# Kernel tuning notes

Hardware: AMD Instinct MI355X
Metric: run time of the kernel (lower is better)

The kernel has to match this reference:

```python
import jax, jax.numpy as jnp
import numpy as np

N_NODES = 50000
N_EDGES = 800000
N_GRAPHS = 64
NUM_CLASSES = 10


def _glorot(key, shape):
    fan_in, fan_out = shape
    lim = np.sqrt(6.0 / (fan_in + fan_out)).astype(np.float32)
    return jax.random.uniform(key, shape, jnp.float32, -lim, lim)


def setup_inputs() -> dict:
    key = jax.random.key(0)
    ks = jax.random.split(key, 12)
    x = jax.random.normal(ks[0], (N_NODES, 5), jnp.float32)
    edge_index = jax.random.randint(ks[1], (2, N_EDGES), 0, N_NODES, jnp.int64)
    batch = jnp.sort(jax.random.randint(ks[2], (N_NODES,), 0, N_GRAPHS, jnp.int64))
    dims = [5, 32, 64, 128, 256]
    params = {}
    for i in range(4):
        params[f"W{i+1}"] = _glorot(ks[3 + i], (dims[i], dims[i + 1]))
        params[f"b{i+1}"] = jnp.zeros((dims[i + 1],), jnp.float32)
    params["fcW"] = _glorot(ks[7], (256, NUM_CLASSES))
    params["fcb"] = jnp.zeros((NUM_CLASSES,), jnp.float32)
    return {"x": x, "edge_index": edge_index, "batch": batch, **params}


def reference(x, edge_index, batch, W1, b1, W2, b2, W3, b3, W4, b4, fcW, fcb):
    n = x.shape[0]
    loop = jnp.arange(n, dtype=edge_index.dtype)
    src = jnp.concatenate([edge_index[0], loop])  # source nodes (+ self loops)
    dst = jnp.concatenate([edge_index[1], loop])  # target nodes (+ self loops)
    # symmetric GCN normalization: D^{-1/2} (A+I) D^{-1/2}
    deg = jax.ops.segment_sum(jnp.ones_like(dst, x.dtype), dst, num_segments=n)
    dinv = jax.lax.rsqrt(deg)  # deg >= 1 due to self loops
    norm = (dinv[src] * dinv[dst])[:, None]

    def gcn(h, W, b):
        h = h @ W                                        # dense transform
        agg = jax.ops.segment_sum(h[src] * norm, dst, num_segments=n)
        return agg + b

    h = jax.nn.relu(gcn(x, W1, b1))
    h = jax.nn.relu(gcn(h, W2, b2))
    h = jax.nn.relu(gcn(h, W3, b3))
    h = jax.nn.relu(gcn(h, W4, b4))                      # [n, 256]

    # global mean pool over graphs
    counts = jax.ops.segment_sum(jnp.ones((n,), h.dtype), batch, num_segments=N_GRAPHS)
    pooled = jax.ops.segment_sum(h, batch, num_segments=N_GRAPHS)
    pooled = pooled / jnp.maximum(counts, 1.0)[:, None]  # [G, 256]

    return jax.nn.log_softmax(pooled @ fcW + fcb, axis=-1)
```

## Files before the change

kernel.cpp:

```cpp
#include <hip/hip_runtime.h>
#include <hip/hip_bf16.h>
#include <math.h>

#define N_NODES 50000
#define N_EDGES 800000
#define N_GRAPHS 64
#define NUM_CLASSES 10
#define BIN_W 256
#define NBINS ((N_NODES + BIN_W - 1) / BIN_W)
#define CHUNK 4096
#define NCHUNKS ((N_EDGES + CHUNK - 1) / CHUNK)
#define CAP 8192
#define CPB 64
#define PACK_BLOCKS 11

typedef __attribute__((ext_vector_type(8))) short bf16x8;
typedef __attribute__((ext_vector_type(4))) float f32x4;

__device__ inline unsigned short f2bf(float f) {
    unsigned int u = __float_as_uint(f);
    u += 0x7fffu + ((u >> 16) & 1u);
    return (unsigned short)(u >> 16);
}
__device__ inline float bf2f(unsigned short v) {
    return __uint_as_float((unsigned int)v << 16);
}
__device__ inline void bf8_unpack(uint4 v, float* o) {
    o[0] = __uint_as_float(v.x << 16); o[1] = __uint_as_float(v.x & 0xffff0000u);
    o[2] = __uint_as_float(v.y << 16); o[3] = __uint_as_float(v.y & 0xffff0000u);
    o[4] = __uint_as_float(v.z << 16); o[5] = __uint_as_float(v.z & 0xffff0000u);
    o[6] = __uint_as_float(v.w << 16); o[7] = __uint_as_float(v.w & 0xffff0000u);
}
__device__ inline unsigned int pack2(float a, float b) {
    return (unsigned int)f2bf(a) | ((unsigned int)f2bf(b) << 16);
}

template<int K, int N>
__device__ void packW_dev(const float* __restrict__ W, unsigned short* __restrict__ Wp,
                          int bid, int l) {
    constexpr int KT = K / 32;
    int kt = bid % KT, nt = bid / KT;
    int m = l & 15, quad = l >> 4;
    #pragma unroll
    for (int j = 0; j < 8; j++) {
        int k = kt * 32 + quad * 8 + j;
        int n = nt * 16 + m;
        Wp[((size_t)bid * 64 + l) * 8 + j] = f2bf(W[(size_t)k * N + n]);
    }
}

__global__ __launch_bounds__(512) void k_binscatter(const int* __restrict__ src,
                                                    const int* __restrict__ dst,
                                                    unsigned short* __restrict__ cnt,
                                                    unsigned int* __restrict__ binned,
                                                    const float* __restrict__ W2,
                                                    const float* __restrict__ W3,
                                                    const float* __restrict__ W4,
                                                    unsigned short* wp2, unsigned short* wp3,
                                                    unsigned short* wp4) {
    int bid = blockIdx.x, t = threadIdx.x;
    if (bid >= NCHUNKS) {
        int w = (bid - NCHUNKS) * 8 + (t >> 6);
        int lane = t & 63;
        if (w < 4)       packW_dev<32, 64>(W2, wp2, w, lane);
        else if (w < 20) packW_dev<64, 128>(W3, wp3, w - 4, lane);
        else if (w < 84) packW_dev<128, 256>(W4, wp4, w - 20, lane);
        return;
    }
    __shared__ int hist[NBINS];
    __shared__ int off[NBINS];
    __shared__ int bump[NBINS];
    __shared__ unsigned int stage[CHUNK];
    __shared__ unsigned char sbin[CHUNK];
    __shared__ int ws8[8];
    int base = bid * CHUNK;
    int total = N_EDGES - base; if (total > CHUNK) total = CHUNK;
    for (int i = t; i < NBINS; i += 512) { hist[i] = 0; bump[i] = 0; }
    __syncthreads();
    int es[8], ed[8];
    #pragma unroll
    for (int i = 0; i < 8; i++) {
        int e = base + t + i * 512;
        if (e < N_EDGES) { es[i] = src[e]; ed[i] = dst[e]; }
        else ed[i] = -1;
    }
    #pragma unroll
    for (int i = 0; i < 8; i++)
        if (ed[i] >= 0) atomicAdd(&hist[ed[i] >> 8], 1);
    __syncthreads();
    {
        int v = (t < NBINS) ? hist[t] : 0;
        int h0 = v;
        int lane = t & 63, w = t >> 6;
        #pragma unroll
        for (int o = 1; o < 64; o <<= 1) { int u = __shfl_up(v, o); if (lane >= o) v += u; }
        if (lane == 63) ws8[w] = v;
        __syncthreads();
        int add = 0;
        #pragma unroll
        for (int i = 0; i < 8; i++) add += (i < w) ? ws8[i] : 0;
        if (t < NBINS) off[t] = v + add - h0;
        __syncthreads();
    }
    #pragma unroll
    for (int i = 0; i < 8; i++) {
        if (ed[i] >= 0) {
            int b = ed[i] >> 8;
            int lpos = off[b] + atomicAdd(&bump[b], 1);
            stage[lpos] = ((unsigned int)(ed[i] & 255) << 16) | (unsigned int)es[i];
            sbin[lpos] = (unsigned char)b;
        }
    }
    __syncthreads();
    for (int j = t; j < total; j += 512) {
        int b = sbin[j];
        int pos = j - off[b];
        if (pos < CPB)
            binned[((size_t)b * NCHUNKS + bid) * CPB + pos] = stage[j];
    }
    if (t < NBINS) {
        int h = hist[t]; if (h > CPB) h = CPB;
        cnt[(size_t)bid * NBINS + t] = (unsigned short)h;
    }
}

__global__ __launch_bounds__(512) void k_csr(const unsigned int* __restrict__ binned,
                                             const unsigned short* __restrict__ cnt,
                                             unsigned int* __restrict__ row_ptr,
                                             float* __restrict__ dinv,
                                             unsigned short* __restrict__ csr16,
                                             const float* __restrict__ x,
                                             float* __restrict__ x5) {
    __shared__ unsigned int stage[CAP];
    __shared__ int coff[256];
    __shared__ unsigned short mycs[256];
    __shared__ int deg[BIN_W];
    __shared__ int off[BIN_W];
    __shared__ int bump[BIN_W];
    __shared__ int ws8[8];
    __shared__ int s_total;
    int b = blockIdx.x;
    int t = threadIdx.x;
    if (t < BIN_W) { deg[t] = 0; bump[t] = 0; }
    int myc = (t < NCHUNKS) ? (int)cnt[(size_t)t * NBINS + b] : 0;
    {
        int v = myc;
        int lane = t & 63, w = t >> 6;
        #pragma unroll
        for (int o = 1; o < 64; o <<= 1) { int u = __shfl_up(v, o); if (lane >= o) v += u; }
        if (lane == 63) ws8[w] = v;
        __syncthreads();
        int add = 0;
        #pragma unroll
        for (int i = 0; i < 8; i++) add += (i < w) ? ws8[i] : 0;
        if (t < 256) { coff[t] = v + add - myc; mycs[t] = (unsigned short)myc; }
        if (t == 511) s_total = v + add;
        __syncthreads();
    }
    int total = s_total; if (total > CAP) total = CAP;
    for (int c = t >> 4; c < NCHUNKS; c += 32) {
        int mc = mycs[c];
        const unsigned int* seg = &binned[((size_t)b * NCHUNKS + c) * CPB];
        int o0 = coff[c];
        for (int j = t & 15; j < mc && o0 + j < CAP; j += 16)
            stage[o0 + j] = seg[j];
    }
    __syncthreads();
    for (int e = t; e < total; e += 512)
        atomicAdd(&deg[stage[e] >> 16], 1);
    __syncthreads();
    {
        int v = (t < BIN_W) ? deg[t] : 0;
        int d0 = v;
        int lane = t & 63, w = t >> 6;
        #pragma unroll
        for (int o = 1; o < 64; o <<= 1) { int u = __shfl_up(v, o); if (lane >= o) v += u; }
        if (lane == 63) ws8[w] = v;
        __syncthreads();
        int add = 0;
        #pragma unroll
        for (int i = 0; i < 8; i++) add += (i < w) ? ws8[i] : 0;
        if (t < BIN_W) off[t] = v + add - d0;
        __syncthreads();
    }
    int e0 = b * CAP;
    if (t < BIN_W) {
        int node = b * BIN_W + t;
        if (node < N_NODES) {
            float di = rsqrtf((float)(deg[t] + 1));
            row_ptr[node] = (unsigned int)(e0 + off[t]) | ((unsigned int)deg[t] << 21);
            dinv[node] = di;
            #pragma unroll
            for (int f = 0; f < 5; f++)
                x5[node * 5 + f] = di * x[node * 5 + f];
        }
    }
    for (int e = t; e < total; e += 512) {
        unsigned int v = stage[e];
        int dl = v >> 16;
        int pos = e0 + off[dl] + atomicAdd(&bump[dl], 1);
        csr16[pos] = (unsigned short)(v & 0xffffu);
    }
}

__global__ __launch_bounds__(256) void k_layer1(const float* __restrict__ x5,
                                                const unsigned int* __restrict__ row_ptr,
                                                const unsigned short* __restrict__ csr16,
                                                const float* __restrict__ dinv,
                                                const float* __restrict__ W1,
                                                const float* __restrict__ b1,
                                                unsigned short* __restrict__ Hout) {
    __shared__ float A5[32 * 6];
    __shared__ float Ws[160];
    __shared__ float bs[32];
    int t = threadIdx.x;
    int row0 = blockIdx.x * 32;
    if (t < 160) Ws[t] = W1[t];
    if (t >= 224) bs[t - 224] = b1[t - 224];
    int nl = t >> 3, f = t & 7;
    int node = row0 + nl;
    float val = 0.0f;
    float dnode = 0.0f;
    if (node < N_NODES) dnode = dinv[node];
    if (f < 5 && node < N_NODES) {
        float acc0 = x5[node * 5 + f], acc1 = 0.0f;
        unsigned int v = row_ptr[node];
        int e0 = (int)(v & 0x1FFFFFu);
        int e1 = e0 + (int)(v >> 21);
        int e = e0;
        for (; e + 7 < e1; e += 8) {
            int s0 = csr16[e], s1 = csr16[e + 1], s2 = csr16[e + 2], s3 = csr16[e + 3];
            int s4 = csr16[e + 4], s5 = csr16[e + 5], s6 = csr16[e + 6], s7 = csr16[e + 7];
            float x0 = x5[s0 * 5 + f], x1 = x5[s1 * 5 + f];
            float x2 = x5[s2 * 5 + f], x3 = x5[s3 * 5 + f];
            float x4 = x5[s4 * 5 + f], x5v = x5[s5 * 5 + f];
            float x6 = x5[s6 * 5 + f], x7 = x5[s7 * 5 + f];
            acc0 += (x0 + x2) + (x4 + x6);
            acc1 += (x1 + x3) + (x5v + x7);
        }
        for (; e + 3 < e1; e += 4) {
            int s0 = csr16[e], s1 = csr16[e + 1], s2 = csr16[e + 2], s3 = csr16[e + 3];
            float x0 = x5[s0 * 5 + f], x1 = x5[s1 * 5 + f];
            float x2 = x5[s2 * 5 + f], x3 = x5[s3 * 5 + f];
            acc0 += x0 + x2;
            acc1 += x1 + x3;
        }
        for (; e < e1; e++) acc0 += x5[csr16[e] * 5 + f];
        val = dnode * (acc0 + acc1);
    }
    if (f < 5) A5[nl * 6 + f] = val;
    __syncthreads();
    int j0 = (t & 7) * 4;
    int node2 = row0 + (t >> 3);
    float d2 = (node2 < N_NODES) ? dinv[node2] : 0.0f;
    float a[5];
    #pragma unroll
    for (int k = 0; k < 5; k++) a[k] = A5[(t >> 3) * 6 + k];
    ushort4 o;
    unsigned short* op = (unsigned short*)&o;
    #pragma unroll
    for (int c = 0; c < 4; c++) {
        float acc = bs[j0 + c];
        #pragma unroll
        for (int k = 0; k < 5; k++) acc += a[k] * Ws[k * 32 + j0 + c];
        op[c] = f2bf(d2 * fmaxf(acc, 0.0f));
    }
    if (node2 < N_NODES) *(ushort4*)&Hout[(size_t)node2 * 32 + j0] = o;
}

template<int K, int N, bool SCALE, bool POOL>
__global__ __launch_bounds__(256) void k_fused(const unsigned short* __restrict__ Hin,
                                               const unsigned int* __restrict__ row_ptr,
                                               const unsigned short* __restrict__ csr16,
                                               const float* __restrict__ dinv,
                                               const unsigned short* __restrict__ Wp,
                                               const float* __restrict__ bias,
                                               unsigned short* __restrict__ C,
                                               const int* __restrict__ batch,
                                               float* __restrict__ pooled) {
    constexpr int KT = K / 32, NT = N / 16, DV = K / 8;
    constexpr int NPB = 2048 / K;
    constexpr int TM = NPB / 16;
    constexpr int KP = K + 8;
    __shared__ unsigned short As[NPB * KP];
    __shared__ int bb[POOL ? NPB : 4];
    int t = threadIdx.x;
    int row0 = blockIdx.x * NPB;
    if constexpr (POOL) {
        if (t < NPB) bb[t] = batch[min(row0 + t, N_NODES - 1)];
    }
    {
        int nl = t / DV, f = t % DV;
        int node = row0 + nl;
        const uint4* h4 = (const uint4*)Hin;
        uint4 o = {0u, 0u, 0u, 0u};
        if (node < N_NODES) {
            float di = dinv[node];
            float acc0[8], acc1[8];
            bf8_unpack(h4[(size_t)node * DV + f], acc0);
            #pragma unroll
            for (int i = 0; i < 8; i++) acc1[i] = 0.0f;
            unsigned int rv = row_ptr[node];
            int e0 = (int)(rv & 0x1FFFFFu);
            int e1 = e0 + (int)(rv >> 21);
            int e = e0;
            for (; e + 3 < e1; e += 4) {
                int s0 = csr16[e], s1 = csr16[e + 1], s2 = csr16[e + 2], s3 = csr16[e + 3];
                uint4 u0 = h4[(size_t)s0 * DV + f];
                uint4 u1 = h4[(size_t)s1 * DV + f];
                uint4 u2 = h4[(size_t)s2 * DV + f];
                uint4 u3 = h4[(size_t)s3 * DV + f];
                float t0[8], t1[8], t2[8], t3[8];
                bf8_unpack(u0, t0); bf8_unpack(u1, t1);
                bf8_unpack(u2, t2); bf8_unpack(u3, t3);
                #pragma unroll
                for (int i = 0; i < 8; i++) {
                    acc0[i] += t0[i] + t2[i];
                    acc1[i] += t1[i] + t3[i];
                }
            }
            for (; e + 1 < e1; e += 2) {
                int s0 = csr16[e], s1 = csr16[e + 1];
                uint4 u0 = h4[(size_t)s0 * DV + f];
                uint4 u1 = h4[(size_t)s1 * DV + f];
                float t0[8], t1[8];
                bf8_unpack(u0, t0);
                bf8_unpack(u1, t1);
                #pragma unroll
                for (int i = 0; i < 8; i++) { acc0[i] += t0[i]; acc1[i] += t1[i]; }
            }
            if (e < e1) {
                float t0[8];
                bf8_unpack(h4[(size_t)csr16[e] * DV + f], t0);
                #pragma unroll
                for (int i = 0; i < 8; i++) acc0[i] += t0[i];
            }
            o.x = pack2(di * (acc0[0] + acc1[0]), di * (acc0[1] + acc1[1]));
            o.y = pack2(di * (acc0[2] + acc1[2]), di * (acc0[3] + acc1[3]));
            o.z = pack2(di * (acc0[4] + acc1[4]), di * (acc0[5] + acc1[5]));
            o.w = pack2(di * (acc0[6] + acc1[6]), di * (acc0[7] + acc1[7]));
        }
        *(uint4*)&As[nl * KP + f * 8] = o;
    }
    __syncthreads();
    int wave = t >> 6, lane = t & 63;
    int m = lane & 15, quad = lane >> 4;
    bf16x8 a[TM][KT];
    float dr[TM][4];
    #pragma unroll
    for (int mt = 0; mt < TM; mt++) {
        #pragma unroll
        for (int kt = 0; kt < KT; kt++)
            a[mt][kt] = *(const bf16x8*)&As[(mt * 16 + m) * KP + kt * 32 + quad * 8];
        #pragma unroll
        for (int r = 0; r < 4; r++) {
            int row = row0 + mt * 16 + quad * 4 + r;
            dr[mt][r] = (SCALE && row < N_NODES) ? dinv[row] : 1.0f;
        }
    }
    const bf16x8* Bp = (const bf16x8*)Wp;
    int g0 = 0, g1 = 0;
    if constexpr (POOL) { g0 = bb[0]; g1 = bb[NPB - 1]; }
    for (int j = wave; j < TM * NT; j += 4) {
        int mt = j % TM, nt = j / TM;
        f32x4 c = {0.f, 0.f, 0.f, 0.f};
        #pragma unroll
        for (int kt = 0; kt < KT; kt++)
            c = __builtin_amdgcn_mfma_f32_16x16x32_bf16(a[mt][kt],
                    Bp[(size_t)(nt * KT + kt) * 64 + lane], c, 0, 0, 0);
        int col = nt * 16 + m;
        float bv = bias[col];
        if constexpr (POOL) {
            float acc0 = 0.0f, acc1 = 0.0f;
            #pragma unroll
            for (int r = 0; r < 4; r++) {
                int rl = mt * 16 + quad * 4 + r;
                int row = row0 + rl;
                if (row < N_NODES) {
                    float v = fmaxf(c[r] + bv, 0.0f);
                    int g = bb[rl];
                    if (g == g0) acc0 += v;
                    else if (g == g1) acc1 += v;
                    else atomicAdd(&pooled[(size_t)g * 256 + col], v);
                }
            }
            acc0 += __shfl_xor(acc0, 32); acc0 += __shfl_xor(acc0, 16);
            acc1 += __shfl_xor(acc1, 32); acc1 += __shfl_xor(acc1, 16);
            if (lane < 16) {
                atomicAdd(&pooled[(size_t)g0 * 256 + col], acc0);
                if (g1 != g0) atomicAdd(&pooled[(size_t)g1 * 256 + col], acc1);
            }
        } else {
            #pragma unroll
            for (int r = 0; r < 4; r++) {
                int row = row0 + mt * 16 + quad * 4 + r;
                if (row < N_NODES) {
                    float v = fmaxf(c[r] + bv, 0.0f);
                    if constexpr (SCALE) v *= dr[mt][r];
                    C[(size_t)row * N + col] = f2bf(v);
                }
            }
        }
    }
}

__global__ void k_final(const float* __restrict__ pooled, const int* __restrict__ batch,
                        const float* __restrict__ fcW, const float* __restrict__ fcb,
                        float* __restrict__ out) {
    int g = blockIdx.x;
    int t = threadIdx.x;
    float cnt = 0.0f;
    if (t == 0) {
        int lo = 0, hi = N_NODES;
        while (lo < hi) { int m = (lo + hi) >> 1; if (batch[m] < g) lo = m + 1; else hi = m; }
        int start = lo;
        lo = 0; hi = N_NODES;
        while (lo < hi) { int m = (lo + hi) >> 1; if (batch[m] < g + 1) lo = m + 1; else hi = m; }
        cnt = (float)(lo - start);
    }
    float inv = 1.0f / fmaxf(__shfl(cnt, 0), 1.0f);
    float p[4];
    #pragma unroll
    for (int m = 0; m < 4; m++) p[m] = pooled[g * 256 + t + 64 * m];
    float logits[NUM_CLASSES];
    #pragma unroll
    for (int j = 0; j < NUM_CLASSES; j++) {
        float s = 0.0f;
        #pragma unroll
        for (int m = 0; m < 4; m++) s += p[m] * fcW[(t + 64 * m) * NUM_CLASSES + j];
        for (int off = 32; off > 0; off >>= 1) s += __shfl_xor(s, off);
        logits[j] = s * inv + fcb[j];
    }
    float mx = logits[0];
    #pragma unroll
    for (int j = 1; j < NUM_CLASSES; j++) mx = fmaxf(mx, logits[j]);
    float se = 0.0f;
    #pragma unroll
    for (int j = 0; j < NUM_CLASSES; j++) se += expf(logits[j] - mx);
    float lse = mx + logf(se);
    if (t < NUM_CLASSES) out[g * NUM_CLASSES + t] = logits[t] - lse;
}

extern "C" void kernel_launch(void* const* d_in, const int* in_sizes, int n_in,
                              void* d_out, int out_size, void* d_ws, size_t ws_size,
                              hipStream_t stream) {
    const float* x     = (const float*)d_in[0];
    const int*   ei    = (const int*)d_in[1];
    const int*   src   = ei;
    const int*   dst   = ei + N_EDGES;
    const int*   batch = (const int*)d_in[2];
    const float* W1 = (const float*)d_in[3];  const float* b1 = (const float*)d_in[4];
    const float* W2 = (const float*)d_in[5];  const float* b2 = (const float*)d_in[6];
    const float* W3 = (const float*)d_in[7];  const float* b3 = (const float*)d_in[8];
    const float* W4 = (const float*)d_in[9];  const float* b4 = (const float*)d_in[10];
    const float* fcW = (const float*)d_in[11]; const float* fcb = (const float*)d_in[12];
    float* out = (float*)d_out;

    char* ws = (char*)d_ws;
    unsigned short* buf1 = (unsigned short*)ws; ws += (size_t)N_NODES * 256 * 2;
    unsigned short* buf2 = (unsigned short*)ws; ws += (size_t)N_NODES * 256 * 2;
    float* dinv     = (float*)ws; ws += (size_t)N_NODES * 4;
    float* x5       = (float*)ws; ws += (size_t)N_NODES * 5 * 4 + 16;
    unsigned int* row_ptr = (unsigned int*)ws; ws += (size_t)(N_NODES + 4) * 4;
    unsigned short* csr16 = (unsigned short*)ws; ws += (size_t)NBINS * CAP * 2;
    unsigned int* binned = (unsigned int*)ws; ws += (size_t)NBINS * NCHUNKS * CPB * 4;
    unsigned short* cnt = (unsigned short*)ws; ws += (size_t)NCHUNKS * NBINS * 2 + 16;
    float* pooled   = (float*)ws; ws += (size_t)N_GRAPHS * 256 * 4;
    unsigned short* wp2 = (unsigned short*)ws; ws += 32 * 64 * 2;
    unsigned short* wp3 = (unsigned short*)ws; ws += 64 * 128 * 2;
    unsigned short* wp4 = (unsigned short*)ws; ws += 128 * 256 * 2;

    const int TB = 256;
    k_binscatter<<<NCHUNKS + PACK_BLOCKS, 512, 0, stream>>>(src, dst, cnt, binned,
                                                            W2, W3, W4, wp2, wp3, wp4);
    k_csr<<<NBINS, 512, 0, stream>>>(binned, cnt, row_ptr, dinv, csr16, x, x5);

    k_layer1<<<(N_NODES + 31) / 32, TB, 0, stream>>>(x5, row_ptr, csr16, dinv, W1, b1, buf1);
    k_fused<32, 64, true, false><<<(N_NODES + 63) / 64, TB, 0, stream>>>(
        buf1, row_ptr, csr16, dinv, wp2, b2, buf2, nullptr, nullptr);
    k_fused<64, 128, true, false><<<(N_NODES + 31) / 32, TB, 0, stream>>>(
        buf2, row_ptr, csr16, dinv, wp3, b3, buf1, nullptr, nullptr);
    k_fused<128, 256, false, true><<<(N_NODES + 15) / 16, TB, 0, stream>>>(
        buf1, row_ptr, csr16, dinv, wp4, b4, nullptr, batch, pooled);

    k_final<<<N_GRAPHS, 64, 0, stream>>>(pooled, batch, fcW, fcb, out);
}
```

Before: 190.5 us.

## Merge pipeline into two persistent cooperative kernels with grid-wide syncs

Replaces the seven separate kernel launches with two cooperative persistent kernels. One does binning, weight packing and CSR construction; the other runs all four GCN layers plus the final classifier, with grid.sync between stages. Blocks loop over work chunks sized by occupancy queries. This removes launch gaps and inter-kernel drain, but adds grid-barrier cost, caps concurrency at resident blocks, and moves the final head onto a single block.

```diff
diff --git a/kernel.cpp b/kernel.cpp
--- a/kernel.cpp
+++ b/kernel.cpp
@@ -1,6 +1,9 @@
 #include <hip/hip_runtime.h>
+#include <hip/hip_cooperative_groups.h>
 #include <hip/hip_bf16.h>
 #include <math.h>
+
+namespace cg = cooperative_groups;
 
 #define N_NODES 50000
 #define N_EDGES 800000
@@ -12,7 +15,7 @@
 #define NCHUNKS ((N_EDGES + CHUNK - 1) / CHUNK)
 #define CAP 8192
 #define CPB 64
-#define PACK_BLOCKS 11
+#define PREP_JOBS (NCHUNKS + 11)
 
 typedef __attribute__((ext_vector_type(8))) short bf16x8;
 typedef __attribute__((ext_vector_type(4))) float f32x4;
@@ -21,9 +24,6 @@
     unsigned int u = __float_as_uint(f);
     u += 0x7fffu + ((u >> 16) & 1u);
     return (unsigned short)(u >> 16);
-}
-__device__ inline float bf2f(unsigned short v) {
-    return __uint_as_float((unsigned int)v << 16);
 }
 __device__ inline void bf8_unpack(uint4 v, float* o) {
     o[0] = __uint_as_float(v.x << 16); o[1] = __uint_as_float(v.x & 0xffff0000u);
@@ -49,174 +49,166 @@
     }
 }
 
-__global__ __launch_bounds__(512) void k_binscatter(const int* __restrict__ src,
-                                                    const int* __restrict__ dst,
-                                                    unsigned short* __restrict__ cnt,
-                                                    unsigned int* __restrict__ binned,
-                                                    const float* __restrict__ W2,
-                                                    const float* __restrict__ W3,
-                                                    const float* __restrict__ W4,
-                                                    unsigned short* wp2, unsigned short* wp3,
-                                                    unsigned short* wp4) {
-    int bid = blockIdx.x, t = threadIdx.x;
-    if (bid >= NCHUNKS) {
-        int w = (bid - NCHUNKS) * 8 + (t >> 6);
-        int lane = t & 63;
-        if (w < 4)       packW_dev<32, 64>(W2, wp2, w, lane);
-        else if (w < 20) packW_dev<64, 128>(W3, wp3, w - 4, lane);
-        else if (w < 84) packW_dev<128, 256>(W4, wp4, w - 20, lane);
-        return;
-    }
-    __shared__ int hist[NBINS];
-    __shared__ int off[NBINS];
-    __shared__ int bump[NBINS];
-    __shared__ unsigned int stage[CHUNK];
-    __shared__ unsigned char sbin[CHUNK];
-    __shared__ int ws8[8];
-    int base = bid * CHUNK;
-    int total = N_EDGES - base; if (total > CHUNK) total = CHUNK;
-    for (int i = t; i < NBINS; i += 512) { hist[i] = 0; bump[i] = 0; }
-    __syncthreads();
-    int es[8], ed[8];
-    #pragma unroll
-    for (int i = 0; i < 8; i++) {
-        int e = base + t + i * 512;
-        if (e < N_EDGES) { es[i] = src[e]; ed[i] = dst[e]; }
-        else ed[i] = -1;
-    }
-    #pragma unroll
-    for (int i = 0; i < 8; i++)
-        if (ed[i] >= 0) atomicAdd(&hist[ed[i] >> 8], 1);
-    __syncthreads();
-    {
-        int v = (t < NBINS) ? hist[t] : 0;
-        int h0 = v;
-        int lane = t & 63, w = t >> 6;
-        #pragma unroll
-        for (int o = 1; o < 64; o <<= 1) { int u = __shfl_up(v, o); if (lane >= o) v += u; }
-        if (lane == 63) ws8[w] = v;
+__global__ __launch_bounds__(512) void k_prep(const int* __restrict__ src,
+                                              const int* __restrict__ dst,
+                                              unsigned short* __restrict__ cnt,
+                                              unsigned int* __restrict__ binned,
+                                              const float* __restrict__ W2,
+                                              const float* __restrict__ W3,
+                                              const float* __restrict__ W4,
+                                              unsigned short* wp2, unsigned short* wp3,
+                                              unsigned short* wp4,
+                                              unsigned int* __restrict__ row_ptr,
+                                              float* __restrict__ dinv,
+                                              unsigned short* __restrict__ csr16,
+                                              const float* __restrict__ x,
+                                              float* __restrict__ x5) {
+    int t = threadIdx.x;
+    __shared__ union SU {
+        struct {
+            int hist[NBINS]; int off[NBINS]; int bump[NBINS];
+            unsigned int stage[CHUNK]; unsigned char sbin[CHUNK]; int ws8[8];
+        } a;
+        struct {
+            unsigned int stage[CAP]; int coff[256]; unsigned short mycs[256];
+            int deg[BIN_W]; int off[BIN_W]; int bump[BIN_W]; int ws8[8]; int s_total;
+        } b;
+    } sm;
+    for (int job = blockIdx.x; job < PREP_JOBS; job += gridDim.x) {
+        if (job >= NCHUNKS) {
+            int w = (job - NCHUNKS) * 8 + (t >> 6);
+            int lane = t & 63;
+            if (w < 4)       packW_dev<32, 64>(W2, wp2, w, lane);
+            else if (w < 20) packW_dev<64, 128>(W3, wp3, w - 4, lane);
+            else if (w < 84) packW_dev<128, 256>(W4, wp4, w - 20, lane);
+        } else {
+            int bid = job;
+            int base = bid * CHUNK;
+            int total = N_EDGES - base; if (total > CHUNK) total = CHUNK;
+            for (int i = t; i < NBINS; i += 512) { sm.a.hist[i] = 0; sm.a.bump[i] = 0; }
+            __syncthreads();
+            int es[8], ed[8];
+            #pragma unroll
+            for (int i = 0; i < 8; i++) {
+                int e = base + t + i * 512;
+                if (e < N_EDGES) { es[i] = src[e]; ed[i] = dst[e]; }
+                else ed[i] = -1;
+            }
+            #pragma unroll
+            for (int i = 0; i < 8; i++)
+                if (ed[i] >= 0) atomicAdd(&sm.a.hist[ed[i] >> 8], 1);
+            __syncthreads();
+            {
+                int v = (t < NBINS) ? sm.a.hist[t] : 0;
+                int h0 = v;
+                int lane = t & 63, w = t >> 6;
+                #pragma unroll
+                for (int o = 1; o < 64; o <<= 1) { int u = __shfl_up(v, o); if (lane >= o) v += u; }
+                if (lane == 63) sm.a.ws8[w] = v;
+                __syncthreads();
+                int add = 0;
+                #pragma unroll
+                for (int i = 0; i < 8; i++) add += (i < w) ? sm.a.ws8[i] : 0;
+                if (t < NBINS) sm.a.off[t] = v + add - h0;
+                __syncthreads();
+            }
+            #pragma unroll
+            for (int i = 0; i < 8; i++) {
+                if (ed[i] >= 0) {
+                    int b = ed[i] >> 8;
+                    int lpos = sm.a.off[b] + atomicAdd(&sm.a.bump[b], 1);
+                    sm.a.stage[lpos] = ((unsigned int)(ed[i] & 255) << 16) | (unsigned int)es[i];
+                    sm.a.sbin[lpos] = (unsigned char)b;
+                }
+            }
+            __syncthreads();
+            for (int j = t; j < total; j += 512) {
+                int b = sm.a.sbin[j];
+                int pos = j - sm.a.off[b];
+                if (pos < CPB)
+                    binned[((size_t)b * NCHUNKS + bid) * CPB + pos] = sm.a.stage[j];
+            }
+            if (t < NBINS) {
+                int h = sm.a.hist[t]; if (h > CPB) h = CPB;
+                cnt[(size_t)bid * NBINS + t] = (unsigned short)h;
+            }
+        }
         __syncthreads();
-        int add = 0;
-        #pragma unroll
-        for (int i = 0; i < 8; i++) add += (i < w) ? ws8[i] : 0;
-        if (t < NBINS) off[t] = v + add - h0;
+    }
+    cg::this_grid().sync();
+    for (int b = blockIdx.x; b < NBINS; b += gridDim.x) {
+        if (t < BIN_W) { sm.b.deg[t] = 0; sm.b.bump[t] = 0; }
+        int myc = (t < NCHUNKS) ? (int)cnt[(size_t)t * NBINS + b] : 0;
+        {
+            int v = myc;
+            int lane = t & 63, w = t >> 6;
+            #pragma unroll
+            for (int o = 1; o < 64; o <<= 1) { int u = __shfl_up(v, o); if (lane >= o) v += u; }
+            if (lane == 63) sm.b.ws8[w] = v;
+            __syncthreads();
+            int add = 0;
+            #pragma unroll
+            for (int i = 0; i < 8; i++) add += (i < w) ? sm.b.ws8[i] : 0;
+            if (t < 256) { sm.b.coff[t] = v + add - myc; sm.b.mycs[t] = (unsigned short)myc; }
+            if (t == 511) sm.b.s_total = v + add;
+            __syncthreads();
+        }
+        int total = sm.b.s_total; if (total > CAP) total = CAP;
+        for (int c = t >> 4; c < NCHUNKS; c += 32) {
+            int mc = sm.b.mycs[c];
+            const unsigned int* seg = &binned[((size_t)b * NCHUNKS + c) * CPB];
+            int o0 = sm.b.coff[c];
+            for (int j = t & 15; j < mc && o0 + j < CAP; j += 16)
+                sm.b.stage[o0 + j] = seg[j];
+        }
         __syncthreads();
-    }
-    #pragma unroll
-    for (int i = 0; i < 8; i++) {
-        if (ed[i] >= 0) {
-            int b = ed[i] >> 8;
-            int lpos = off[b] + atomicAdd(&bump[b], 1);
-            stage[lpos] = ((unsigned int)(ed[i] & 255) << 16) | (unsigned int)es[i];
-            sbin[lpos] = (unsigned char)b;
-        }
-    }
-    __syncthreads();
-    for (int j = t; j < total; j += 512) {
-        int b = sbin[j];
-        int pos = j - off[b];
-        if (pos < CPB)
-            binned[((size_t)b * NCHUNKS + bid) * CPB + pos] = stage[j];
-    }
-    if (t < NBINS) {
-        int h = hist[t]; if (h > CPB) h = CPB;
-        cnt[(size_t)bid * NBINS + t] = (unsigned short)h;
-    }
-}
-
-__global__ __launch_bounds__(512) void k_csr(const unsigned int* __restrict__ binned,
-                                             const unsigned short* __restrict__ cnt,
-                                             unsigned int* __restrict__ row_ptr,
-                                             float* __restrict__ dinv,
-                                             unsigned short* __restrict__ csr16,
-                                             const float* __restrict__ x,
-                                             float* __restrict__ x5) {
-    __shared__ unsigned int stage[CAP];
-    __shared__ int coff[256];
-    __shared__ unsigned short mycs[256];
-    __shared__ int deg[BIN_W];
-    __shared__ int off[BIN_W];
-    __shared__ int bump[BIN_W];
-    __shared__ int ws8[8];
-    __shared__ int s_total;
-    int b = blockIdx.x;
-    int t = threadIdx.x;
-    if (t < BIN_W) { deg[t] = 0; bump[t] = 0; }
-    int myc = (t < NCHUNKS) ? (int)cnt[(size_t)t * NBINS + b] : 0;
-    {
-        int v = myc;
-        int lane = t & 63, w = t >> 6;
-        #pragma unroll
-        for (int o = 1; o < 64; o <<= 1) { int u = __shfl_up(v, o); if (lane >= o) v += u; }
-        if (lane == 63) ws8[w] = v;
+        for (int e = t; e < total; e += 512)
+            atomicAdd(&sm.b.deg[sm.b.stage[e] >> 16], 1);
         __syncthreads();
-        int add = 0;
-        #pragma unroll
-        for (int i = 0; i < 8; i++) add += (i < w) ? ws8[i] : 0;
-        if (t < 256) { coff[t] = v + add - myc; mycs[t] = (unsigned short)myc; }
-        if (t == 511) s_total = v + add;
+        {
+            int v = (t < BIN_W) ? sm.b.deg[t] : 0;
+            int d0 = v;
+            int lane = t & 63, w = t >> 6;
+            #pragma unroll
+            for (int o = 1; o < 64; o <<= 1) { int u = __shfl_up(v, o); if (lane >= o) v += u; }
+            if (lane == 63) sm.b.ws8[w] = v;
+            __syncthreads();
+            int add = 0;
+            #pragma unroll
+            for (int i = 0; i < 8; i++) add += (i < w) ? sm.b.ws8[i] : 0;
+            if (t < BIN_W) sm.b.off[t] = v + add - d0;
+            __syncthreads();
+        }
+        int e0 = b * CAP;
+        if (t < BIN_W) {
+            int node = b * BIN_W + t;
+            if (node < N_NODES) {
+                float di = rsqrtf((float)(sm.b.deg[t] + 1));
+                row_ptr[node] = (unsigned int)(e0 + sm.b.off[t]) | ((unsigned int)sm.b.deg[t] << 21);
+                dinv[node] = di;
+                #pragma unroll
+                for (int f = 0; f < 5; f++)
+                    x5[node * 5 + f] = di * x[node * 5 + f];
+            }
+        }
+        for (int e = t; e < total; e += 512) {
+            unsigned int v = sm.b.stage[e];
+            int dl = v >> 16;
+            int pos = e0 + sm.b.off[dl] + atomicAdd(&sm.b.bump[dl], 1);
+            csr16[pos] = (unsigned short)(v & 0xffffu);
+        }
         __syncthreads();
     }
-    int total = s_total; if (total > CAP) total = CAP;
-    for (int c = t >> 4; c < NCHUNKS; c += 32) {
-        int mc = mycs[c];
-        const unsigned int* seg = &binned[((size_t)b * NCHUNKS + c) * CPB];
-        int o0 = coff[c];
-        for (int j = t & 15; j < mc && o0 + j < CAP; j += 16)
-            stage[o0 + j] = seg[j];
-    }
-    __syncthreads();
-    for (int e = t; e < total; e += 512)
-        atomicAdd(&deg[stage[e] >> 16], 1);
-    __syncthreads();
-    {
-        int v = (t < BIN_W) ? deg[t] : 0;
-        int d0 = v;
-        int lane = t & 63, w = t >> 6;
-        #pragma unroll
-        for (int o = 1; o < 64; o <<= 1) { int u = __shfl_up(v, o); if (lane >= o) v += u; }
-        if (lane == 63) ws8[w] = v;
-        __syncthreads();
-        int add = 0;
-        #pragma unroll
-        for (int i = 0; i < 8; i++) add += (i < w) ? ws8[i] : 0;
-        if (t < BIN_W) off[t] = v + add - d0;
-        __syncthreads();
-    }
-    int e0 = b * CAP;
-    if (t < BIN_W) {
-        int node = b * BIN_W + t;
-        if (node < N_NODES) {
-            float di = rsqrtf((float)(deg[t] + 1));
-            row_ptr[node] = (unsigned int)(e0 + off[t]) | ((unsigned int)deg[t] << 21);
-            dinv[node] = di;
-            #pragma unroll
-            for (int f = 0; f < 5; f++)
-                x5[node * 5 + f] = di * x[node * 5 + f];
-        }
-    }
-    for (int e = t; e < total; e += 512) {
-        unsigned int v = stage[e];
-        int dl = v >> 16;
-        int pos = e0 + off[dl] + atomicAdd(&bump[dl], 1);
-        csr16[pos] = (unsigned short)(v & 0xffffu);
-    }
-}
-
-__global__ __launch_bounds__(256) void k_layer1(const float* __restrict__ x5,
-                                                const unsigned int* __restrict__ row_ptr,
-                                                const unsigned short* __restrict__ csr16,
-                                                const float* __restrict__ dinv,
-                                                const float* __restrict__ W1,
-                                                const float* __restrict__ b1,
-                                                unsigned short* __restrict__ Hout) {
-    __shared__ float A5[32 * 6];
-    __shared__ float Ws[160];
-    __shared__ float bs[32];
-    int t = threadIdx.x;
-    int row0 = blockIdx.x * 32;
-    if (t < 160) Ws[t] = W1[t];
-    if (t >= 224) bs[t - 224] = b1[t - 224];
+}
+
+__device__ __forceinline__ void layer1_chunk(int c, const float* __restrict__ x5,
+                                             const unsigned int* __restrict__ row_ptr,
+                                             const unsigned short* __restrict__ csr16,
+                                             const float* __restrict__ dinv,
+                                             const float* Ws, const float* bs,
+                                             unsigned short* __restrict__ Hout,
+                                             float* A5, int t) {
+    int row0 = c * 32;
     int nl = t >> 3, f = t & 7;
     int node = row0 + nl;
     float val = 0.0f;
@@ -259,33 +251,32 @@
     ushort4 o;
     unsigned short* op = (unsigned short*)&o;
     #pragma unroll
-    for (int c = 0; c < 4; c++) {
-        float acc = bs[j0 + c];
+    for (int cc = 0; cc < 4; cc++) {
+        float acc = bs[j0 + cc];
         #pragma unroll
-        for (int k = 0; k < 5; k++) acc += a[k] * Ws[k * 32 + j0 + c];
-        op[c] = f2bf(d2 * fmaxf(acc, 0.0f));
+        for (int k = 0; k < 5; k++) acc += a[k] * Ws[k * 32 + j0 + cc];
+        op[cc] = f2bf(d2 * fmaxf(acc, 0.0f));
     }
     if (node2 < N_NODES) *(ushort4*)&Hout[(size_t)node2 * 32 + j0] = o;
+    __syncthreads();
 }
 
 template<int K, int N, bool SCALE, bool POOL>
-__global__ __launch_bounds__(256) void k_fused(const unsigned short* __restrict__ Hin,
-                                               const unsigned int* __restrict__ row_ptr,
-                                               const unsigned short* __restrict__ csr16,
-                                               const float* __restrict__ dinv,
-                                               const unsigned short* __restrict__ Wp,
-                                               const float* __restrict__ bias,
-                                               unsigned short* __restrict__ C,
-                                               const int* __restrict__ batch,
-                                               float* __restrict__ pooled) {
+__device__ __forceinline__ void fused_chunk(int blk, const unsigned short* __restrict__ Hin,
+                                            const unsigned int* __restrict__ row_ptr,
+                                            const unsigned short* __restrict__ csr16,
+                                            const float* __restrict__ dinv,
+                                            const unsigned short* __restrict__ Wp,
+                                            const float* __restrict__ bias,
+                                            unsigned short* __restrict__ C,
+                                            const int* __restrict__ batch,
+                                            float* __restrict__ pooled,
+                                            unsigned short* As, int* bb, int t) {
     constexpr int KT = K / 32, NT = N / 16, DV = K / 8;
     constexpr int NPB = 2048 / K;
     constexpr int TM = NPB / 16;
     constexpr int KP = K + 8;
-    __shared__ unsigned short As[NPB * KP];
-    __shared__ int bb[POOL ? NPB : 4];
-    int t = threadIdx.x;
-    int row0 = blockIdx.x * NPB;
+    int row0 = blk * NPB;
     if constexpr (POOL) {
         if (t < NPB) bb[t] = batch[min(row0 + t, N_NODES - 1)];
     }
@@ -402,43 +393,88 @@
             }
         }
     }
-}
-
-__global__ void k_final(const float* __restrict__ pooled, const int* __restrict__ batch,
-                        const float* __restrict__ fcW, const float* __restrict__ fcb,
-                        float* __restrict__ out) {
-    int g = blockIdx.x;
+    __syncthreads();
+}
+
+__global__ __launch_bounds__(256) void k_layers(const float* __restrict__ x5,
+                                                const unsigned int* __restrict__ row_ptr,
+                                                const unsigned short* __restrict__ csr16,
+                                                const float* __restrict__ dinv,
+                                                const float* __restrict__ W1,
+                                                const float* __restrict__ b1,
+                                                unsigned short* __restrict__ buf1,
+                                                unsigned short* __restrict__ buf2,
+                                                const unsigned short* __restrict__ wp2,
+                                                const float* __restrict__ b2,
+                                                const unsigned short* __restrict__ wp3,
+                                                const float* __restrict__ b3,
+                                                const unsigned short* __restrict__ wp4,
+                                                const float* __restrict__ b4,
+                                                const int* __restrict__ batch,
+                                                float* __restrict__ pooled,
+                                                const float* __restrict__ fcW,
+                                                const float* __restrict__ fcb,
+                                                float* __restrict__ out) {
+    cg::grid_group grid = cg::this_grid();
     int t = threadIdx.x;
-    float cnt = 0.0f;
-    if (t == 0) {
-        int lo = 0, hi = N_NODES;
-        while (lo < hi) { int m = (lo + hi) >> 1; if (batch[m] < g) lo = m + 1; else hi = m; }
-        int start = lo;
-        lo = 0; hi = N_NODES;
-        while (lo < hi) { int m = (lo + hi) >> 1; if (batch[m] < g + 1) lo = m + 1; else hi = m; }
-        cnt = (float)(lo - start);
-    }
-    float inv = 1.0f / fmaxf(__shfl(cnt, 0), 1.0f);
-    float p[4];
-    #pragma unroll
-    for (int m = 0; m < 4; m++) p[m] = pooled[g * 256 + t + 64 * m];
-    float logits[NUM_CLASSES];
-    #pragma unroll
-    for (int j = 0; j < NUM_CLASSES; j++) {
-        float s = 0.0f;
-        #pragma unroll
-        for (int m = 0; m < 4; m++) s += p[m] * fcW[(t + 64 * m) * NUM_CLASSES + j];
-        for (int off = 32; off > 0; off >>= 1) s += __shfl_xor(s, off);
-        logits[j] = s * inv + fcb[j];
-    }
-    float mx = logits[0];
-    #pragma unroll
-    for (int j = 1; j < NUM_CLASSES; j++) mx = fmaxf(mx, logits[j]);
-    float se = 0.0f;
-    #pragma unroll
-    for (int j = 0; j < NUM_CLASSES; j++) se += expf(logits[j] - mx);
-    float lse = mx + logf(se);
-    if (t < NUM_CLASSES) out[g * NUM_CLASSES + t] = logits[t] - lse;
+    __shared__ unsigned short As[64 * 40];
+    __shared__ int bb[64];
+    __shared__ float A5[32 * 6];
+    __shared__ float Ws[160];
+    __shared__ float bs[32];
+    if (t < 160) Ws[t] = W1[t];
+    if (t >= 224) bs[t - 224] = b1[t - 224];
+    __syncthreads();
+    for (int c = blockIdx.x; c < (N_NODES + 31) / 32; c += gridDim.x)
+        layer1_chunk(c, x5, row_ptr, csr16, dinv, Ws, bs, buf1, A5, t);
+    grid.sync();
+    for (int c = blockIdx.x; c < (N_NODES + 63) / 64; c += gridDim.x)
+        fused_chunk<32, 64, true, false>(c, buf1, row_ptr, csr16, dinv, wp2, b2,
+                                         buf2, nullptr, nullptr, As, bb, t);
+    grid.sync();
+    for (int c = blockIdx.x; c < (N_NODES + 31) / 32; c += gridDim.x)
+        fused_chunk<64, 128, true, false>(c, buf2, row_ptr, csr16, dinv, wp3, b3,
+                                          buf1, nullptr, nullptr, As, bb, t);
+    grid.sync();
+    for (int c = blockIdx.x; c < (N_NODES + 15) / 16; c += gridDim.x)
+        fused_chunk<128, 256, false, true>(c, buf1, row_ptr, csr16, dinv, wp4, b4,
+                                           nullptr, batch, pooled, As, bb, t);
+    grid.sync();
+    if (blockIdx.x == 0) {
+        int w = t >> 6, l = t & 63;
+        for (int g = w; g < N_GRAPHS; g += 4) {
+            float cntf = 0.0f;
+            if (l == 0) {
+                int lo = 0, hi = N_NODES;
+                while (lo < hi) { int mm = (lo + hi) >> 1; if (batch[mm] < g) lo = mm + 1; else hi = mm; }
+                int start = lo;
+                lo = 0; hi = N_NODES;
+                while (lo < hi) { int mm = (lo + hi) >> 1; if (batch[mm] < g + 1) lo = mm + 1; else hi = mm; }
+                cntf = (float)(lo - start);
+            }
+            float inv = 1.0f / fmaxf(__shfl(cntf, 0), 1.0f);
+            float p[4];
+            #pragma unroll
+            for (int m = 0; m < 4; m++) p[m] = pooled[g * 256 + l + 64 * m];
+            float logits[NUM_CLASSES];
+            #pragma unroll
+            for (int j = 0; j < NUM_CLASSES; j++) {
+                float s = 0.0f;
+                #pragma unroll
+                for (int m = 0; m < 4; m++) s += p[m] * fcW[(l + 64 * m) * NUM_CLASSES + j];
+                for (int off = 32; off > 0; off >>= 1) s += __shfl_xor(s, off);
+                logits[j] = s * inv + fcb[j];
+            }
+            float mx = logits[0];
+            #pragma unroll
+            for (int j = 1; j < NUM_CLASSES; j++) mx = fmaxf(mx, logits[j]);
+            float se = 0.0f;
+            #pragma unroll
+            for (int j = 0; j < NUM_CLASSES; j++) se += expf(logits[j] - mx);
+            float lse = mx + logf(se);
+            if (l < NUM_CLASSES) out[g * NUM_CLASSES + l] = logits[l] - lse;
+        }
+    }
 }
 
 extern "C" void kernel_launch(void* const* d_in, const int* in_sizes, int n_in,
@@ -470,18 +506,30 @@
     unsigned short* wp3 = (unsigned short*)ws; ws += 64 * 128 * 2;
     unsigned short* wp4 = (unsigned short*)ws; ws += 128 * 256 * 2;
 
-    const int TB = 256;
-    k_binscatter<<<NCHUNKS + PACK_BLOCKS, 512, 0, stream>>>(src, dst, cnt, binned,
-                                                            W2, W3, W4, wp2, wp3, wp4);
-    k_csr<<<NBINS, 512, 0, stream>>>(binned, cnt, row_ptr, dinv, csr16, x, x5);
-
-    k_layer1<<<(N_NODES + 31) / 32, TB, 0, stream>>>(x5, row_ptr, csr16, dinv, W1, b1, buf1);
-    k_fused<32, 64, true, false><<<(N_NODES + 63) / 64, TB, 0, stream>>>(
-        buf1, row_ptr, csr16, dinv, wp2, b2, buf2, nullptr, nullptr);
-    k_fused<64, 128, true, false><<<(N_NODES + 31) / 32, TB, 0, stream>>>(
-        buf2, row_ptr, csr16, dinv, wp3, b3, buf1, nullptr, nullptr);
-    k_fused<128, 256, false, true><<<(N_NODES + 15) / 16, TB, 0, stream>>>(
-        buf1, row_ptr, csr16, dinv, wp4, b4, nullptr, batch, pooled);
-
-    k_final<<<N_GRAPHS, 64, 0, stream>>>(pooled, batch, fcW, fcb, out);
-}
+    static int gA = 0, gB = 0;
+    if (gA == 0) {
+        int occ = 1;
+        hipOccupancyMaxActiveBlocksPerMultiprocessor(&occ, (const void*)k_prep, 512, 0);
+        if (occ < 1) occ = 1;
+        long long g = (long long)occ * 256;
+        gA = (int)(g > PREP_JOBS ? PREP_JOBS : g);
+        occ = 1;
+        hipOccupancyMaxActiveBlocksPerMultiprocessor(&occ, (const void*)k_layers, 256, 0);
+        if (occ < 1) occ = 1;
+        g = (long long)occ * 256;
+        gB = (int)(g > 3125 ? 3125 : g);
+    }
+
+    void* aA[] = {(void*)&src, (void*)&dst, (void*)&cnt, (void*)&binned,
+                  (void*)&W2, (void*)&W3, (void*)&W4,
+                  (void*)&wp2, (void*)&wp3, (void*)&wp4,
+                  (void*)&row_ptr, (void*)&dinv, (void*)&csr16, (void*)&x, (void*)&x5};
+    hipLaunchCooperativeKernel((const void*)k_prep, dim3(gA), dim3(512), aA, 0, stream);
+
+    void* aB[] = {(void*)&x5, (void*)&row_ptr, (void*)&csr16, (void*)&dinv,
+                  (void*)&W1, (void*)&b1, (void*)&buf1, (void*)&buf2,
+                  (void*)&wp2, (void*)&b2, (void*)&wp3, (void*)&b3,
+                  (void*)&wp4, (void*)&b4, (void*)&batch, (void*)&pooled,
+                  (void*)&fcW, (void*)&fcb, (void*)&out};
+    hipLaunchCooperativeKernel((const void*)k_layers, dim3(gB), dim3(256), aB, 0, stream);
+}
```

Result: slower. 638.3 us (+235.1%).
